# Optimization experiments

Hardware: AMD Instinct MI355X
Metric: run time of the kernel (lower is better)

Reference implementation:

```python
import jax, jax.numpy as jnp
import numpy as np

N = 2048

def setup_inputs() -> dict:
    key = jax.random.key(0)
    kx, kq, kk, kv = jax.random.split(key, 4)
    x = jax.random.normal(kx, (N, N), dtype=jnp.float32)
    q = jax.random.normal(kq, (N, N), dtype=jnp.float32)
    k = jax.random.normal(kk, (N, N), dtype=jnp.float32)
    v = jax.random.normal(kv, (N, N), dtype=jnp.float32)
    return {"x": x, "q": q, "k": k, "v": v}

def reference(x, q, k, v):
    # qk = (x @ q) @ (x @ k)  -- note: NOT (x@k).T, faithful to torch.mm chain
    qk = jnp.matmul(jnp.matmul(x, q), jnp.matmul(x, k))  # [n, n]
    attn = jax.nn.softmax(qk, axis=-1)                   # row softmax over n
    return jnp.matmul(attn, jnp.matmul(x, v))            # [n, n]
```

## Files before the change

kernel.cpp:

```cpp
#include <hip/hip_runtime.h>
#include <stdint.h>


#define TN 2048

typedef float f32x4 __attribute__((ext_vector_type(4)));
typedef _Float16 f16;
typedef f16 f16x8 __attribute__((ext_vector_type(8)));
typedef f16 f16x4 __attribute__((ext_vector_type(4)));

#define MFMA16(a, b, c) __builtin_amdgcn_mfma_f32_16x16x32_f16(a, b, c, 0, 0, 0)
#define SBAR() asm volatile("s_barrier" ::: "memory")
#define VMCNT(n) asm volatile("s_waitcnt vmcnt(" #n ")" ::: "memory")

__device__ __forceinline__ void glds16(const f16* g, f16* l) {
    __builtin_amdgcn_global_load_lds(
        (const __attribute__((address_space(1))) unsigned int*)g,
        (__attribute__((address_space(3))) unsigned int*)l, 16, 0, 0);
}

__global__ void split2_kernel(const float* __restrict__ in,
                              f16* __restrict__ t0, f16* __restrict__ t1) {
    int i = (blockIdx.x * 256 + threadIdx.x) * 4;
    f32x4 f = *(const f32x4*)(in + i);
    f16x4 o0, o1;
#pragma unroll
    for (int e = 0; e < 4; ++e) {
        float a = f[e];
        f16 h0 = (f16)a;
        o0[e] = h0; o1[e] = (f16)(a - (float)h0);
    }
    *(f16x4*)(t0 + i) = o0; *(f16x4*)(t1 + i) = o1;
}

__global__ void split2_add_kernel(const float* __restrict__ inA,
                                  const float* __restrict__ inB,
                                  f16* __restrict__ t0, f16* __restrict__ t1) {
    int i = (blockIdx.x * 256 + threadIdx.x) * 4;
    f32x4 fa = *(const f32x4*)(inA + i);
    f32x4 fb = *(const f32x4*)(inB + i);
    f16x4 o0, o1;
#pragma unroll
    for (int e = 0; e < 4; ++e) {
        float a = fa[e] + fb[e];
        f16 h0 = (f16)a;
        o0[e] = h0; o1[e] = (f16)(a - (float)h0);
    }
    *(f16x4*)(t0 + i) = o0; *(f16x4*)(t1 + i) = o1;
}

__global__ void split2t_kernel(const float* __restrict__ in,
                               f16* __restrict__ t0, f16* __restrict__ t1) {
    __shared__ f16 s0[64][68], s1[64][68];
    int bc = blockIdx.x * 64, br = blockIdx.y * 64;
    int tx = threadIdx.x & 15, ty = threadIdx.x >> 4;
#pragma unroll
    for (int rr = 0; rr < 64; rr += 16) {
        int r = rr + ty;
        f32x4 f = *(const f32x4*)(in + (size_t)(br + r) * TN + bc + tx * 4);
#pragma unroll
        for (int e = 0; e < 4; ++e) {
            float a = f[e];
            f16 h0 = (f16)a;
            s0[tx * 4 + e][r] = h0; s1[tx * 4 + e][r] = (f16)(a - (float)h0);
        }
    }
    __syncthreads();
#pragma unroll
    for (int rr = 0; rr < 64; rr += 16) {
        int c = rr + ty;
        f16x4 o0, o1;
#pragma unroll
        for (int e = 0; e < 4; ++e) { o0[e] = s0[c][tx*4+e]; o1[e] = s1[c][tx*4+e]; }
        size_t off = (size_t)(bc + c) * TN + br + tx * 4;
        *(f16x4*)(t0 + off) = o0; *(f16x4*)(t1 + off) = o1;
    }
}

__global__ void split2t_add_kernel(const float* __restrict__ inA,
                                   const float* __restrict__ inB,
                                   f16* __restrict__ t0, f16* __restrict__ t1) {
    __shared__ f16 s0[64][68], s1[64][68];
    int bc = blockIdx.x * 64, br = blockIdx.y * 64;
    int tx = threadIdx.x & 15, ty = threadIdx.x >> 4;
#pragma unroll
    for (int rr = 0; rr < 64; rr += 16) {
        int r = rr + ty;
        size_t off = (size_t)(br + r) * TN + bc + tx * 4;
        f32x4 fa = *(const f32x4*)(inA + off);
        f32x4 fb = *(const f32x4*)(inB + off);
#pragma unroll
        for (int e = 0; e < 4; ++e) {
            float a = fa[e] + fb[e];
            f16 h0 = (f16)a;
            s0[tx * 4 + e][r] = h0; s1[tx * 4 + e][r] = (f16)(a - (float)h0);
        }
    }
    __syncthreads();
#pragma unroll
    for (int rr = 0; rr < 64; rr += 16) {
        int c = rr + ty;
        f16x4 o0, o1;
#pragma unroll
        for (int e = 0; e < 4; ++e) { o0[e] = s0[c][tx*4+e]; o1[e] = s1[c][tx*4+e]; }
        size_t off = (size_t)(bc + c) * TN + br + tx * 4;
        *(f16x4*)(t0 + off) = o0; *(f16x4*)(t1 + off) = o1;
    }
}

__global__ void cast1t_kernel(const float* __restrict__ in, f16* __restrict__ t0) {
    __shared__ f16 s0[64][68];
    int bc = blockIdx.x * 64, br = blockIdx.y * 64;
    int tx = threadIdx.x & 15, ty = threadIdx.x >> 4;
#pragma unroll
    for (int rr = 0; rr < 64; rr += 16) {
        int r = rr + ty;
        f32x4 f = *(const f32x4*)(in + (size_t)(br + r) * TN + bc + tx * 4);
#pragma unroll
        for (int e = 0; e < 4; ++e) s0[tx * 4 + e][r] = (f16)f[e];
    }
    __syncthreads();
#pragma unroll
    for (int rr = 0; rr < 64; rr += 16) {
        int c = rr + ty;
        f16x4 o0;
#pragma unroll
        for (int e = 0; e < 4; ++e) o0[e] = s0[c][tx*4+e];
        *(f16x4*)(t0 + (size_t)(bc + c) * TN + br + tx * 4) = o0;
    }
}

__global__ void cast1t_add_kernel(const float* __restrict__ inA,
                                  const float* __restrict__ inB,
                                  f16* __restrict__ t0) {
    __shared__ f16 s0[64][68];
    int bc = blockIdx.x * 64, br = blockIdx.y * 64;
    int tx = threadIdx.x & 15, ty = threadIdx.x >> 4;
#pragma unroll
    for (int rr = 0; rr < 64; rr += 16) {
        int r = rr + ty;
        size_t off = (size_t)(br + r) * TN + bc + tx * 4;
        f32x4 fa = *(const f32x4*)(inA + off);
        f32x4 fb = *(const f32x4*)(inB + off);
#pragma unroll
        for (int e = 0; e < 4; ++e) s0[tx * 4 + e][r] = (f16)(fa[e] + fb[e]);
    }
    __syncthreads();
#pragma unroll
    for (int rr = 0; rr < 64; rr += 16) {
        int c = rr + ty;
        f16x4 o0;
#pragma unroll
        for (int e = 0; e < 4; ++e) o0[e] = s0[c][tx*4+e];
        *(f16x4*)(t0 + (size_t)(bc + c) * TN + br + tx * 4) = o0;
    }
}

__global__ void final_add_kernel(const float* __restrict__ inA,
                                 const float* __restrict__ inB,
                                 float* __restrict__ out) {
    int i = (blockIdx.x * 256 + threadIdx.x) * 4;
    f32x4 fa = *(const f32x4*)(inA + i);
    f32x4 fb = *(const f32x4*)(inB + i);
    f32x4 o;
#pragma unroll
    for (int e = 0; e < 4; ++e) o[e] = fa[e] + fb[e];
    *(f32x4*)(out + i) = o;
}

__global__ __launch_bounds__(512, 2) void gemmqk_f16(
    const f16* __restrict__ a0p, const f16* __restrict__ a1p,
    const f16* __restrict__ q0p, const f16* __restrict__ q1p,
    const f16* __restrict__ k0p, const f16* __restrict__ k1p,
    float* __restrict__ Wq0, float* __restrict__ Wq1,
    float* __restrict__ Wk0, float* __restrict__ Wk1) {
    __shared__ f16 lds[2][64 * 512];
    const int tid = threadIdx.x;
    const int wave = tid >> 6, lane = tid & 63;
    const int wrow = wave >> 1, wcol = wave & 1;
    const int quad = lane >> 4, l16 = lane & 15;
    const int bm = blockIdx.y * 256;
    const int bnf = blockIdx.x * 256;
    const int bsel = bnf >= TN;
    const int bc = bnf & (TN - 1);
    const int kbase = blockIdx.z * 1024;
    const f16* __restrict__ b0p = bsel ? k0p : q0p;
    const f16* __restrict__ b1p = bsel ? k1p : q1p;
    float* __restrict__ C = bsel ? (blockIdx.z ? Wk1 : Wk0)
                                 : (blockIdx.z ? Wq1 : Wq0);

    const int ws = wave * 8;
    const f16* sp[8];
#pragma unroll
    for (int t = 0; t < 8; ++t) {
        int s = ws + t;
        const f16* base; int gr;
        if (s < 16)      { base = a0p; gr = bm + s * 16 + l16; }
        else if (s < 32) { base = a1p; gr = bm + (s - 16) * 16 + l16; }
        else if (s < 48) { base = b0p; gr = bc + (s - 32) * 16 + l16; }
        else             { base = b1p; gr = bc + (s - 48) * 16 + l16; }
        sp[t] = base + (size_t)gr * TN + kbase + quad * 8;
    }
    const int rof = lane * 8;
    const int sa0 = wrow * 4,      sa1 = 16 + wrow * 4;
    const int sb0 = 32 + wcol * 8, sb1 = 48 + wcol * 8;

    f32x4 acc[4][8];
#pragma unroll
    for (int i = 0; i < 4; ++i)
#pragma unroll
        for (int j = 0; j < 8; ++j) acc[i][j] = (f32x4){0.f, 0.f, 0.f, 0.f};

#pragma unroll
    for (int t = 0; t < 8; ++t) { glds16(sp[t], &lds[0][(ws + t) * 512]); sp[t] += 32; }
    f16* cur = &lds[0][0]; f16* nxt = &lds[1][0];
    VMCNT(0); SBAR();

    f16x8 a0f[4], a1f[4], b0f[8], b1f[8];
#pragma unroll
    for (int i = 0; i < 4; ++i) a0f[i] = *(const f16x8*)(cur + (sa0 + i) * 512 + rof);
#pragma unroll
    for (int j = 0; j < 8; ++j) b0f[j] = *(const f16x8*)(cur + (sb0 + j) * 512 + rof);

    for (int step = 0; step < 32; ++step) {
#pragma unroll
        for (int i = 0; i < 4; ++i) a1f[i] = *(const f16x8*)(cur + (sa1 + i) * 512 + rof);
        if (step < 31) {
#pragma unroll
            for (int t = 0; t < 8; ++t) { glds16(sp[t], nxt + (ws + t) * 512); sp[t] += 32; }
        }
        SBAR();
        __builtin_amdgcn_s_setprio(1);
#pragma unroll
        for (int i = 0; i < 4; ++i)
#pragma unroll
            for (int j = 0; j < 8; ++j) acc[i][j] = MFMA16(a0f[i], b0f[j], acc[i][j]);
        __builtin_amdgcn_s_setprio(0);
        SBAR();
#pragma unroll
        for (int j = 0; j < 8; ++j) b1f[j] = *(const f16x8*)(cur + (sb1 + j) * 512 + rof);
        SBAR();
        __builtin_amdgcn_s_setprio(1);
#pragma unroll
        for (int i = 0; i < 4; ++i)
#pragma unroll
            for (int j = 0; j < 8; ++j) acc[i][j] = MFMA16(a1f[i], b0f[j], acc[i][j]);
        __builtin_amdgcn_s_setprio(0);
        SBAR();
        __builtin_amdgcn_s_setprio(1);
#pragma unroll
        for (int i = 0; i < 4; ++i)
#pragma unroll
            for (int j = 0; j < 8; ++j) acc[i][j] = MFMA16(a0f[i], b1f[j], acc[i][j]);
        __builtin_amdgcn_s_setprio(0);
        if (step < 31) {
            VMCNT(0);
            SBAR();
#pragma unroll
            for (int i = 0; i < 4; ++i) a0f[i] = *(const f16x8*)(nxt + (sa0 + i) * 512 + rof);
#pragma unroll
            for (int j = 0; j < 8; ++j) b0f[j] = *(const f16x8*)(nxt + (sb0 + j) * 512 + rof);
        }
        f16* tmp = cur; cur = nxt; nxt = tmp;
    }
#pragma unroll
    for (int i = 0; i < 4; ++i)
#pragma unroll
        for (int j = 0; j < 8; ++j) {
            int row = bm + wrow * 64 + i * 16 + quad * 4;
            int col = bc + wcol * 128 + j * 16 + l16;
            float* p = C + (size_t)row * TN + col;
#pragma unroll
            for (int r = 0; r < 4; ++r) p[(size_t)r * TN] = acc[i][j][r];
        }
}

__global__ __launch_bounds__(512, 2) void gemm3_f16(
    const f16* __restrict__ a0p, const f16* __restrict__ a1p,
    const f16* __restrict__ b0p, const f16* __restrict__ b1p,
    float* __restrict__ C0, float* __restrict__ C1) {
    __shared__ f16 lds[3][48 * 512];
    const int tid = threadIdx.x;
    const int wave = tid >> 6, lane = tid & 63;
    const int wrow = wave >> 2, wcol = wave & 3;
    const int quad = lane >> 4, l16 = lane & 15;
    const int bm = blockIdx.y * 128, bn = blockIdx.x * 256;
    const int kbase = blockIdx.z * 1024;
    float* __restrict__ C = blockIdx.z ? C1 : C0;

    const int ws = wave * 6;
    const f16* sp[6];
#pragma unroll
    for (int t = 0; t < 6; ++t) {
        int s = ws + t;
        const f16* base; int gr;
        if (s < 8)       { base = a0p; gr = bm + s * 16 + l16; }
        else if (s < 16) { base = a1p; gr = bm + (s - 8) * 16 + l16; }
        else if (s < 32) { base = b0p; gr = bn + (s - 16) * 16 + l16; }
        else             { base = b1p; gr = bn + (s - 32) * 16 + l16; }
        sp[t] = base + (size_t)gr * TN + kbase + quad * 8;
    }
    const int rof = lane * 8;
    const int sa0 = wrow * 4, sa1 = 8 + wrow * 4;
    const int sb0 = 16 + wcol * 4, sb1 = 32 + wcol * 4;

    f32x4 acc[4][4];
#pragma unroll
    for (int i = 0; i < 4; ++i)
#pragma unroll
        for (int j = 0; j < 4; ++j) acc[i][j] = (f32x4){0.f, 0.f, 0.f, 0.f};

#pragma unroll
    for (int t = 0; t < 6; ++t) { glds16(sp[t], &lds[0][(ws + t) * 512]); sp[t] += 32; }
#pragma unroll
    for (int t = 0; t < 6; ++t) { glds16(sp[t], &lds[1][(ws + t) * 512]); sp[t] += 32; }
    f16* cur = &lds[0][0]; f16* nxt = &lds[1][0]; f16* pre = &lds[2][0];
    VMCNT(6); SBAR();

    f16x8 a0f[4], a1f[4], b0f[4], b1f[4];
#pragma unroll
    for (int i = 0; i < 4; ++i) a0f[i] = *(const f16x8*)(cur + (sa0 + i) * 512 + rof);
#pragma unroll
    for (int j = 0; j < 4; ++j) b0f[j] = *(const f16x8*)(cur + (sb0 + j) * 512 + rof);

    for (int step = 0; step < 32; ++step) {
#pragma unroll
        for (int j = 0; j < 4; ++j) b1f[j] = *(const f16x8*)(cur + (sb1 + j) * 512 + rof);
        if (step < 30) {
#pragma unroll
            for (int t = 0; t < 3; ++t) { glds16(sp[t], pre + (ws + t) * 512); sp[t] += 32; }
        }
        SBAR();
        __builtin_amdgcn_s_setprio(1);
#pragma unroll
        for (int i = 0; i < 4; ++i)
#pragma unroll
            for (int j = 0; j < 4; ++j) acc[i][j] = MFMA16(a0f[i], b0f[j], acc[i][j]);
        __builtin_amdgcn_s_setprio(0);
        SBAR();
#pragma unroll
        for (int i = 0; i < 4; ++i) a1f[i] = *(const f16x8*)(cur + (sa1 + i) * 512 + rof);
        if (step < 30) {
#pragma unroll
            for (int t = 3; t < 6; ++t) { glds16(sp[t], pre + (ws + t) * 512); sp[t] += 32; }
        }
        SBAR();
        __builtin_amdgcn_s_setprio(1);
#pragma unroll
        for (int i = 0; i < 4; ++i)
#pragma unroll
            for (int j = 0; j < 4; ++j) acc[i][j] = MFMA16(a0f[i], b1f[j], acc[i][j]);
        __builtin_amdgcn_s_setprio(0);
        SBAR();
        __builtin_amdgcn_s_setprio(1);
#pragma unroll
        for (int i = 0; i < 4; ++i)
#pragma unroll
            for (int j = 0; j < 4; ++j) acc[i][j] = MFMA16(a1f[i], b0f[j], acc[i][j]);
        __builtin_amdgcn_s_setprio(0);
        if (step < 31) {
            if (step < 30) { VMCNT(6); } else { VMCNT(0); }
            SBAR();
#pragma unroll
            for (int i = 0; i < 4; ++i) a0f[i] = *(const f16x8*)(nxt + (sa0 + i) * 512 + rof);
#pragma unroll
            for (int j = 0; j < 4; ++j) b0f[j] = *(const f16x8*)(nxt + (sb0 + j) * 512 + rof);
        }
        f16* tmp = cur; cur = nxt; nxt = pre; pre = tmp;
    }
#pragma unroll
    for (int i = 0; i < 4; ++i)
#pragma unroll
        for (int j = 0; j < 4; ++j) {
            int row = bm + wrow * 64 + i * 16 + quad * 4;
            int col = bn + wcol * 64 + j * 16 + l16;
            float* p = C + (size_t)row * TN + col;
#pragma unroll
            for (int r = 0; r < 4; ++r) p[(size_t)r * TN] = acc[i][j][r];
        }
}

__global__ __launch_bounds__(256, 2) void gemm1_f16(
    const f16* __restrict__ A, const f16* __restrict__ Bt,
    float* __restrict__ C0, float* __restrict__ C1) {
    __shared__ f16 lds[3][16 * 512];
    const int tid = threadIdx.x;
    const int wave = tid >> 6, lane = tid & 63;
    const int wr = (wave >> 1) * 64, wc = (wave & 1) * 64;
    const int quad = lane >> 4, l16 = lane & 15;
    const int bm = blockIdx.y * 128, bn = blockIdx.x * 128;
    const int kbase = blockIdx.z * 1024;
    float* __restrict__ C = blockIdx.z ? C1 : C0;

    const int ws = wave * 4;
    const f16* sp[4];
#pragma unroll
    for (int t = 0; t < 4; ++t) {
        int s = ws + t;
        const f16* base; int gr;
        if (s < 8) { base = A;  gr = bm + s * 16 + l16; }
        else       { base = Bt; gr = bn + (s - 8) * 16 + l16; }
        sp[t] = base + (size_t)gr * TN + kbase + quad * 8;
    }
    const int rof = lane * 8;
    const int sa = (wr >> 4), sb = 8 + (wc >> 4);

    f32x4 acc[4][4];
#pragma unroll
    for (int i = 0; i < 4; ++i)
#pragma unroll
        for (int j = 0; j < 4; ++j) acc[i][j] = (f32x4){0.f, 0.f, 0.f, 0.f};

#pragma unroll
    for (int t = 0; t < 4; ++t) { glds16(sp[t], &lds[0][(ws + t) * 512]); sp[t] += 32; }
#pragma unroll
    for (int t = 0; t < 4; ++t) { glds16(sp[t], &lds[1][(ws + t) * 512]); sp[t] += 32; }
    f16* cur = &lds[0][0]; f16* nxt = &lds[1][0]; f16* pre = &lds[2][0];
    VMCNT(4); SBAR();

    f16x8 af[4], bf[4];
#pragma unroll
    for (int i = 0; i < 4; ++i) af[i] = *(const f16x8*)(cur + (sa + i) * 512 + rof);
#pragma unroll
    for (int j = 0; j < 4; ++j) bf[j] = *(const f16x8*)(cur + (sb + j) * 512 + rof);

    for (int step = 0; step < 32; ++step) {
        if (step < 30) {
#pragma unroll
            for (int t = 0; t < 4; ++t) { glds16(sp[t], pre + (ws + t) * 512); sp[t] += 32; }
        }
        SBAR();
        __builtin_amdgcn_s_setprio(1);
#pragma unroll
        for (int i = 0; i < 4; ++i)
#pragma unroll
            for (int j = 0; j < 4; ++j) acc[i][j] = MFMA16(af[i], bf[j], acc[i][j]);
        __builtin_amdgcn_s_setprio(0);
        if (step < 31) {
            if (step < 30) { VMCNT(4); } else { VMCNT(0); }
            SBAR();
#pragma unroll
            for (int i = 0; i < 4; ++i) af[i] = *(const f16x8*)(nxt + (sa + i) * 512 + rof);
#pragma unroll
            for (int j = 0; j < 4; ++j) bf[j] = *(const f16x8*)(nxt + (sb + j) * 512 + rof);
        }
        f16* tmp = cur; cur = nxt; nxt = pre; pre = tmp;
    }
#pragma unroll
    for (int i = 0; i < 4; ++i)
#pragma unroll
        for (int j = 0; j < 4; ++j) {
            int row = bm + wr + i * 16 + quad * 4;
            int col = bn + wc + j * 16 + l16;
            float* p = C + (size_t)row * TN + col;
#pragma unroll
            for (int r = 0; r < 4; ++r) p[(size_t)r * TN] = acc[i][j][r];
        }
}

__global__ void softmax_add_kernel(const float* __restrict__ S0,
                                   const float* __restrict__ S1,
                                   f16* __restrict__ P) {
    __shared__ float red[256];
    const int row = blockIdx.x, tid = threadIdx.x;
    const size_t base = (size_t)row * TN + tid * 8;
    f32x4 a0 = *(const f32x4*)(S0 + base);
    f32x4 a1 = *(const f32x4*)(S0 + base + 4);
    f32x4 b0 = *(const f32x4*)(S1 + base);
    f32x4 b1 = *(const f32x4*)(S1 + base + 4);
    float vals[8];
#pragma unroll
    for (int e = 0; e < 4; ++e) { vals[e] = a0[e] + b0[e]; vals[4 + e] = a1[e] + b1[e]; }
    float m = vals[0];
#pragma unroll
    for (int e = 1; e < 8; ++e) m = fmaxf(m, vals[e]);
    red[tid] = m; __syncthreads();
    for (int st = 128; st > 0; st >>= 1) { if (tid < st) red[tid] = fmaxf(red[tid], red[tid + st]); __syncthreads(); }
    m = red[0]; __syncthreads();
    float sum = 0.f;
#pragma unroll
    for (int e = 0; e < 8; ++e) { vals[e] = expf(vals[e] - m); sum += vals[e]; }
    red[tid] = sum; __syncthreads();
    for (int st = 128; st > 0; st >>= 1) { if (tid < st) red[tid] += red[tid + st]; __syncthreads(); }
    float inv = 1.f / red[0];
    f16x8 o;
#pragma unroll
    for (int e = 0; e < 8; ++e) o[e] = (f16)(vals[e] * inv);
    *(f16x8*)(P + base) = o;
}

extern "C" void kernel_launch(void* const* d_in, const int* in_sizes, int n_in,
                              void* d_out, int out_size, void* d_ws, size_t ws_size,
                              hipStream_t stream) {
    const float* x = (const float*)d_in[0];
    const float* q = (const float*)d_in[1];
    const float* k = (const float*)d_in[2];
    const float* v = (const float*)d_in[3];
    float* out = (float*)d_out;
    const size_t M = (size_t)TN * TN;

    float* W1 = (float*)d_ws;
    float* W2 = W1 + M;
    f16* pl = (f16*)(W2 + M);
    f16 *x0 = pl,         *x1 = pl + M;
    f16 *q0 = pl + 2 * M, *q1 = pl + 3 * M;
    f16 *k0 = pl + 4 * M, *k1 = pl + 5 * M;
    f16 *v0 = pl + 6 * M;
    f16 *a0 = q0, *a1 = q1;
    f16 *b0 = k0, *b1 = k1;
    f16 *p0 = x1, *c0 = x0;
    float* W4 = (float*)(pl + 7 * M);
    float* W3 = out;

    dim3 bs(256), bs3(512);
    dim3 gelem(TN * TN / 4 / 256);
    dim3 gt(TN / 64, TN / 64);
    dim3 gg3(TN / 256, TN / 128, 2);
    dim3 ggqk(2 * TN / 256, TN / 256, 2);
    dim3 gg1(TN / 128, TN / 128, 2);

    const size_t need = (size_t)(3 * 4 + 7 * 2) * M;

    hipLaunchKernelGGL(split2_kernel,  gelem, bs, 0, stream, x, x0, x1);
    hipLaunchKernelGGL(cast1t_kernel,  gt,    bs, 0, stream, v, v0);
    hipLaunchKernelGGL(split2t_kernel, gt,    bs, 0, stream, q, q0, q1);

    if (ws_size >= need) {
        hipLaunchKernelGGL(split2t_kernel, gt, bs, 0, stream, k, k0, k1);
        hipLaunchKernelGGL(gemmqk_f16, ggqk, bs3, 0, stream,
                           x0, x1, q0, q1, k0, k1, W1, W2, W3, W4);
        hipLaunchKernelGGL(split2_add_kernel,  gelem, bs, 0, stream, W1, W2, a0, a1);
        hipLaunchKernelGGL(split2t_add_kernel, gt,    bs, 0, stream, W3, W4, b0, b1);
    } else {
        hipLaunchKernelGGL(gemm3_f16, gg3, bs3, 0, stream, x0, x1, q0, q1, W1, W2);
        hipLaunchKernelGGL(split2_add_kernel, gelem, bs, 0, stream, W1, W2, a0, a1);
        hipLaunchKernelGGL(split2t_kernel, gt, bs, 0, stream, k, k0, k1);
        hipLaunchKernelGGL(gemm3_f16, gg3, bs3, 0, stream, x0, x1, k0, k1, W1, W2);
        hipLaunchKernelGGL(split2t_add_kernel, gt, bs, 0, stream, W1, W2, b0, b1);
    }
    hipLaunchKernelGGL(gemm3_f16, gg3, bs3, 0, stream, a0, a1, b0, b1, W1, W2);
    hipLaunchKernelGGL(softmax_add_kernel, dim3(TN), bs, 0, stream, W1, W2, p0);
    hipLaunchKernelGGL(gemm1_f16, gg1, bs, 0, stream, x0, v0, W1, W2);
    hipLaunchKernelGGL(cast1t_add_kernel, gt, bs, 0, stream, W1, W2, c0);
    hipLaunchKernelGGL(gemm1_f16, gg1, bs, 0, stream, p0, c0, W1, W2);
    hipLaunchKernelGGL(final_add_kernel, gelem, bs, 0, stream, W1, W2, out);
}
```

Before: 383.0 us.

## Use 128x256 tiles with 4-way split-K in single-plane GEMMs and fuse q/k/v prep

The single-plane f16 GEMM now uses a 128x256 output tile per block and splits K four ways, 512 each, instead of 128x128 tiles with two-way split-K. The reductions and casts become four-input add kernels. The q/k/v split and cast kernels are merged into one launch with a z-dimension selector, which removes two launches. The change aims to raise data reuse per block and cut launch overhead. In exchange it writes and reads two more fp32 partial buffers and uses more registers per thread for the larger accumulator.

```diff
diff --git a/kernel.cpp b/kernel.cpp
--- a/kernel.cpp
+++ b/kernel.cpp
@@ -49,6 +49,61 @@
     *(f16x4*)(t0 + i) = o0; *(f16x4*)(t1 + i) = o1;
 }
 
+__global__ void prep_qkv_kernel(const float* __restrict__ q,
+                                const float* __restrict__ k,
+                                const float* __restrict__ v,
+                                f16* __restrict__ q0, f16* __restrict__ q1,
+                                f16* __restrict__ k0, f16* __restrict__ k1,
+                                f16* __restrict__ v0) {
+    __shared__ f16 s0[64][68], s1[64][68];
+    int bc = blockIdx.x * 64, br = blockIdx.y * 64;
+    int tx = threadIdx.x & 15, ty = threadIdx.x >> 4;
+    int z = blockIdx.z;
+    if (z < 2) {
+        const float* in = z ? k : q;
+        f16* t0 = z ? k0 : q0;
+        f16* t1 = z ? k1 : q1;
+#pragma unroll
+        for (int rr = 0; rr < 64; rr += 16) {
+            int r = rr + ty;
+            f32x4 f = *(const f32x4*)(in + (size_t)(br + r) * TN + bc + tx * 4);
+#pragma unroll
+            for (int e = 0; e < 4; ++e) {
+                float a = f[e];
+                f16 h0 = (f16)a;
+                s0[tx * 4 + e][r] = h0; s1[tx * 4 + e][r] = (f16)(a - (float)h0);
+            }
+        }
+        __syncthreads();
+#pragma unroll
+        for (int rr = 0; rr < 64; rr += 16) {
+            int c = rr + ty;
+            f16x4 o0, o1;
+#pragma unroll
+            for (int e = 0; e < 4; ++e) { o0[e] = s0[c][tx*4+e]; o1[e] = s1[c][tx*4+e]; }
+            size_t off = (size_t)(bc + c) * TN + br + tx * 4;
+            *(f16x4*)(t0 + off) = o0; *(f16x4*)(t1 + off) = o1;
+        }
+    } else {
+#pragma unroll
+        for (int rr = 0; rr < 64; rr += 16) {
+            int r = rr + ty;
+            f32x4 f = *(const f32x4*)(v + (size_t)(br + r) * TN + bc + tx * 4);
+#pragma unroll
+            for (int e = 0; e < 4; ++e) s0[tx * 4 + e][r] = (f16)f[e];
+        }
+        __syncthreads();
+#pragma unroll
+        for (int rr = 0; rr < 64; rr += 16) {
+            int c = rr + ty;
+            f16x4 o0;
+#pragma unroll
+            for (int e = 0; e < 4; ++e) o0[e] = s0[c][tx*4+e];
+            *(f16x4*)(v0 + (size_t)(bc + c) * TN + br + tx * 4) = o0;
+        }
+    }
+}
+
 __global__ void split2t_kernel(const float* __restrict__ in,
                                f16* __restrict__ t0, f16* __restrict__ t1) {
     __shared__ f16 s0[64][68], s1[64][68];
@@ -144,6 +199,36 @@
         f32x4 fb = *(const f32x4*)(inB + off);
 #pragma unroll
         for (int e = 0; e < 4; ++e) s0[tx * 4 + e][r] = (f16)(fa[e] + fb[e]);
+    }
+    __syncthreads();
+#pragma unroll
+    for (int rr = 0; rr < 64; rr += 16) {
+        int c = rr + ty;
+        f16x4 o0;
+#pragma unroll
+        for (int e = 0; e < 4; ++e) o0[e] = s0[c][tx*4+e];
+        *(f16x4*)(t0 + (size_t)(bc + c) * TN + br + tx * 4) = o0;
+    }
+}
+
+__global__ void cast1t_add4_kernel(const float* __restrict__ inA,
+                                   const float* __restrict__ inB,
+                                   const float* __restrict__ inC,
+                                   const float* __restrict__ inD,
+                                   f16* __restrict__ t0) {
+    __shared__ f16 s0[64][68];
+    int bc = blockIdx.x * 64, br = blockIdx.y * 64;
+    int tx = threadIdx.x & 15, ty = threadIdx.x >> 4;
+#pragma unroll
+    for (int rr = 0; rr < 64; rr += 16) {
+        int r = rr + ty;
+        size_t off = (size_t)(br + r) * TN + bc + tx * 4;
+        f32x4 fa = *(const f32x4*)(inA + off);
+        f32x4 fb = *(const f32x4*)(inB + off);
+        f32x4 fc = *(const f32x4*)(inC + off);
+        f32x4 fd = *(const f32x4*)(inD + off);
+#pragma unroll
+        for (int e = 0; e < 4; ++e) s0[tx * 4 + e][r] = (f16)((fa[e] + fb[e]) + (fc[e] + fd[e]));
     }
     __syncthreads();
 #pragma unroll
@@ -165,6 +250,22 @@
     f32x4 o;
 #pragma unroll
     for (int e = 0; e < 4; ++e) o[e] = fa[e] + fb[e];
+    *(f32x4*)(out + i) = o;
+}
+
+__global__ void final_add4_kernel(const float* __restrict__ inA,
+                                  const float* __restrict__ inB,
+                                  const float* __restrict__ inC,
+                                  const float* __restrict__ inD,
+                                  float* __restrict__ out) {
+    int i = (blockIdx.x * 256 + threadIdx.x) * 4;
+    f32x4 fa = *(const f32x4*)(inA + i);
+    f32x4 fb = *(const f32x4*)(inB + i);
+    f32x4 fc = *(const f32x4*)(inC + i);
+    f32x4 fd = *(const f32x4*)(inD + i);
+    f32x4 o;
+#pragma unroll
+    for (int e = 0; e < 4; ++e) o[e] = (fa[e] + fb[e]) + (fc[e] + fd[e]);
     *(f32x4*)(out + i) = o;
 }
 
@@ -382,6 +483,87 @@
 
 __global__ __launch_bounds__(256, 2) void gemm1_f16(
     const f16* __restrict__ A, const f16* __restrict__ Bt,
+    float* __restrict__ C0, float* __restrict__ C1,
+    float* __restrict__ C2, float* __restrict__ C3) {
+    __shared__ f16 lds[3][24 * 512];
+    const int tid = threadIdx.x;
+    const int wave = tid >> 6, lane = tid & 63;
+    const int wrow = wave >> 1, wcol = wave & 1;
+    const int quad = lane >> 4, l16 = lane & 15;
+    const int bm = blockIdx.y * 128, bn = blockIdx.x * 256;
+    const int kbase = blockIdx.z * 512;
+    const int bz = blockIdx.z;
+    float* __restrict__ C = (bz == 0) ? C0 : (bz == 1) ? C1 : (bz == 2) ? C2 : C3;
+
+    const int ws = wave * 6;
+    const f16* sp[6];
+#pragma unroll
+    for (int t = 0; t < 6; ++t) {
+        int s = ws + t;
+        const f16* base; int gr;
+        if (s < 8) { base = A;  gr = bm + s * 16 + l16; }
+        else       { base = Bt; gr = bn + (s - 8) * 16 + l16; }
+        sp[t] = base + (size_t)gr * TN + kbase + quad * 8;
+    }
+    const int rof = lane * 8;
+    const int sa = wrow * 4;
+    const int sb = 8 + wcol * 8;
+
+    f32x4 acc[4][8];
+#pragma unroll
+    for (int i = 0; i < 4; ++i)
+#pragma unroll
+        for (int j = 0; j < 8; ++j) acc[i][j] = (f32x4){0.f, 0.f, 0.f, 0.f};
+
+#pragma unroll
+    for (int t = 0; t < 6; ++t) { glds16(sp[t], &lds[0][(ws + t) * 512]); sp[t] += 32; }
+#pragma unroll
+    for (int t = 0; t < 6; ++t) { glds16(sp[t], &lds[1][(ws + t) * 512]); sp[t] += 32; }
+    f16* cur = &lds[0][0]; f16* nxt = &lds[1][0]; f16* pre = &lds[2][0];
+    VMCNT(6); SBAR();
+
+    f16x8 af[4], bf[8];
+#pragma unroll
+    for (int i = 0; i < 4; ++i) af[i] = *(const f16x8*)(cur + (sa + i) * 512 + rof);
+#pragma unroll
+    for (int j = 0; j < 8; ++j) bf[j] = *(const f16x8*)(cur + (sb + j) * 512 + rof);
+
+    for (int step = 0; step < 16; ++step) {
+        if (step < 14) {
+#pragma unroll
+            for (int t = 0; t < 6; ++t) { glds16(sp[t], pre + (ws + t) * 512); sp[t] += 32; }
+        }
+        SBAR();
+        __builtin_amdgcn_s_setprio(1);
+#pragma unroll
+        for (int i = 0; i < 4; ++i)
+#pragma unroll
+            for (int j = 0; j < 8; ++j) acc[i][j] = MFMA16(af[i], bf[j], acc[i][j]);
+        __builtin_amdgcn_s_setprio(0);
+        if (step < 15) {
+            if (step < 14) { VMCNT(6); } else { VMCNT(0); }
+            SBAR();
+#pragma unroll
+            for (int i = 0; i < 4; ++i) af[i] = *(const f16x8*)(nxt + (sa + i) * 512 + rof);
+#pragma unroll
+            for (int j = 0; j < 8; ++j) bf[j] = *(const f16x8*)(nxt + (sb + j) * 512 + rof);
+        }
+        f16* tmp = cur; cur = nxt; nxt = pre; pre = tmp;
+    }
+#pragma unroll
+    for (int i = 0; i < 4; ++i)
+#pragma unroll
+        for (int j = 0; j < 8; ++j) {
+            int row = bm + wrow * 64 + i * 16 + quad * 4;
+            int col = bn + wcol * 128 + j * 16 + l16;
+            float* p = C + (size_t)row * TN + col;
+#pragma unroll
+            for (int r = 0; r < 4; ++r) p[(size_t)r * TN] = acc[i][j][r];
+        }
+}
+
+__global__ __launch_bounds__(256, 2) void gemm1_f16_z2(
+    const f16* __restrict__ A, const f16* __restrict__ Bt,
     float* __restrict__ C0, float* __restrict__ C1) {
     __shared__ f16 lds[3][16 * 512];
     const int tid = threadIdx.x;
@@ -515,33 +697,41 @@
     dim3 bs(256), bs3(512);
     dim3 gelem(TN * TN / 4 / 256);
     dim3 gt(TN / 64, TN / 64);
+    dim3 gt3(TN / 64, TN / 64, 3);
     dim3 gg3(TN / 256, TN / 128, 2);
     dim3 ggqk(2 * TN / 256, TN / 256, 2);
-    dim3 gg1(TN / 128, TN / 128, 2);
+    dim3 gg1(TN / 256, TN / 128, 4);
+    dim3 gg1f(TN / 128, TN / 128, 2);
 
     const size_t need = (size_t)(3 * 4 + 7 * 2) * M;
 
-    hipLaunchKernelGGL(split2_kernel,  gelem, bs, 0, stream, x, x0, x1);
-    hipLaunchKernelGGL(cast1t_kernel,  gt,    bs, 0, stream, v, v0);
-    hipLaunchKernelGGL(split2t_kernel, gt,    bs, 0, stream, q, q0, q1);
+    hipLaunchKernelGGL(split2_kernel, gelem, bs, 0, stream, x, x0, x1);
 
     if (ws_size >= need) {
-        hipLaunchKernelGGL(split2t_kernel, gt, bs, 0, stream, k, k0, k1);
+        hipLaunchKernelGGL(prep_qkv_kernel, gt3, bs, 0, stream, q, k, v, q0, q1, k0, k1, v0);
         hipLaunchKernelGGL(gemmqk_f16, ggqk, bs3, 0, stream,
                            x0, x1, q0, q1, k0, k1, W1, W2, W3, W4);
         hipLaunchKernelGGL(split2_add_kernel,  gelem, bs, 0, stream, W1, W2, a0, a1);
         hipLaunchKernelGGL(split2t_add_kernel, gt,    bs, 0, stream, W3, W4, b0, b1);
+        hipLaunchKernelGGL(gemm3_f16, gg3, bs3, 0, stream, a0, a1, b0, b1, W1, W2);
+        hipLaunchKernelGGL(softmax_add_kernel, dim3(TN), bs, 0, stream, W1, W2, p0);
+        hipLaunchKernelGGL(gemm1_f16, gg1, bs, 0, stream, x0, v0, W1, W2, out, W4);
+        hipLaunchKernelGGL(cast1t_add4_kernel, gt, bs, 0, stream, W1, W2, out, W4, c0);
+        hipLaunchKernelGGL(gemm1_f16, gg1, bs, 0, stream, p0, c0, out, W1, W2, W4);
+        hipLaunchKernelGGL(final_add4_kernel, gelem, bs, 0, stream, out, W1, W2, W4, out);
     } else {
+        hipLaunchKernelGGL(cast1t_kernel,  gt, bs, 0, stream, v, v0);
+        hipLaunchKernelGGL(split2t_kernel, gt, bs, 0, stream, q, q0, q1);
         hipLaunchKernelGGL(gemm3_f16, gg3, bs3, 0, stream, x0, x1, q0, q1, W1, W2);
         hipLaunchKernelGGL(split2_add_kernel, gelem, bs, 0, stream, W1, W2, a0, a1);
         hipLaunchKernelGGL(split2t_kernel, gt, bs, 0, stream, k, k0, k1);
         hipLaunchKernelGGL(gemm3_f16, gg3, bs3, 0, stream, x0, x1, k0, k1, W1, W2);
         hipLaunchKernelGGL(split2t_add_kernel, gt, bs, 0, stream, W1, W2, b0, b1);
-    }
-    hipLaunchKernelGGL(gemm3_f16, gg3, bs3, 0, stream, a0, a1, b0, b1, W1, W2);
-    hipLaunchKernelGGL(softmax_add_kernel, dim3(TN), bs, 0, stream, W1, W2, p0);
-    hipLaunchKernelGGL(gemm1_f16, gg1, bs, 0, stream, x0, v0, W1, W2);
-    hipLaunchKernelGGL(cast1t_add_kernel, gt, bs, 0, stream, W1, W2, c0);
-    hipLaunchKernelGGL(gemm1_f16, gg1, bs, 0, stream, p0, c0, W1, W2);
-    hipLaunchKernelGGL(final_add_kernel, gelem, bs, 0, stream, W1, W2, out);
-}
+        hipLaunchKernelGGL(gemm3_f16, gg3, bs3, 0, stream, a0, a1, b0, b1, W1, W2);
+        hipLaunchKernelGGL(softmax_add_kernel, dim3(TN), bs, 0, stream, W1, W2, p0);
+        hipLaunchKernelGGL(gemm1_f16_z2, gg1f, bs, 0, stream, x0, v0, W1, W2);
+        hipLaunchKernelGGL(cast1t_add_kernel, gt, bs, 0, stream, W1, W2, c0);
+        hipLaunchKernelGGL(gemm1_f16_z2, gg1f, bs, 0, stream, p0, c0, W1, W2);
+        hipLaunchKernelGGL(final_add_kernel, gelem, bs, 0, stream, W1, W2, out);
+    }
+}
```

Result: no change. 388.4 us (+1.4%).
